# Kernel optimization log

Hardware: AMD Instinct MI355X
Metric: run time of the kernel (lower is better)

The kernel has to match this reference:

```python
import jax, jax.numpy as jnp
import numpy as np

B, S, HID = 2, 2048, 768
NH, HD = 12, 64  # num heads, head dim


def setup_inputs() -> dict:
    key = jax.random.key(0)
    ks = jax.random.split(key, 10)
    scale = 0.02
    return {
        "hidden_states": jax.random.normal(ks[0], (B, S, HID), jnp.float32),
        "rel_pos": jax.random.normal(ks[1], (B, NH, S, S), jnp.float32),
        "rel_2d_pos": jax.random.normal(ks[2], (B, NH, S, S), jnp.float32),
        "attention_mask": jax.random.randint(ks[3], (B, 1, S, S), 0, 2, jnp.int32),
        "Wq": jax.random.normal(ks[4], (HID, HID), jnp.float32) * scale,
        "bq": jnp.zeros((HID,), jnp.float32),
        "Wk": jax.random.normal(ks[5], (HID, HID), jnp.float32) * scale,
        "bk": jnp.zeros((HID,), jnp.float32),
        "Wv": jax.random.normal(ks[6], (HID, HID), jnp.float32) * scale,
        "bv": jnp.zeros((HID,), jnp.float32),
    }


def _heads(x):
    # [B,S,HID] -> [B,NH,S,HD]
    return x.reshape(B, S, NH, HD).transpose(0, 2, 1, 3)


def reference(hidden_states, rel_pos, rel_2d_pos, attention_mask, Wq, bq, Wk, bk, Wv, bv):
    q = _heads(hidden_states @ Wq.T + bq) / jnp.sqrt(jnp.asarray(HD, hidden_states.dtype))
    k = _heads(hidden_states @ Wk.T + bk)
    v = _heads(hidden_states @ Wv.T + bv)
    scores = jnp.einsum('bhsd,bhtd->bhst', q, k)
    scores = scores + rel_pos + rel_2d_pos
    scores = jnp.where(attention_mask.astype(bool), jnp.finfo(jnp.float32).min, scores.astype(jnp.float32))
    probs = jax.nn.softmax(scores, axis=-1).astype(v.dtype)
    ctx = jnp.einsum('bhst,bhtd->bhsd', probs, v)
    return ctx.transpose(0, 2, 1, 3).reshape(B, S, HID)
```

## Files before the change

### kernel.cpp

```cpp
#include <hip/hip_runtime.h>

#define B_ 2
#define S_ 2048
#define HID_ 768
#define NH_ 12
#define HD_ 64
#define NSPLIT 2
#define KSPAN (S_ / NSPLIT)
#define NROWS (B_ * NH_ * S_)

typedef unsigned short u16;
typedef __attribute__((ext_vector_type(8))) short bf16x8;
typedef __attribute__((ext_vector_type(4))) float f32x4;

static __device__ inline u16 f2bf(float f) {
    union { float f; unsigned u; } v; v.f = f;
    unsigned r = v.u + 0x7fffu + ((v.u >> 16) & 1u);
    return (u16)(r >> 16);
}

#define LDS_BARRIER() asm volatile("s_waitcnt lgkmcnt(0)\n\ts_barrier" ::: "memory")

__global__ void cast_bf16(const float* __restrict__ src, u16* __restrict__ dst, int n) {
    int i = (blockIdx.x * blockDim.x + threadIdx.x) * 4;
    if (i < n) {
        float4 v = *(const float4*)(src + i);
        unsigned lo = (unsigned)f2bf(v.x) | ((unsigned)f2bf(v.y) << 16);
        unsigned hi = (unsigned)f2bf(v.z) | ((unsigned)f2bf(v.w) << 16);
        uint2 o; o.x = lo; o.y = hi;
        *(uint2*)(dst + i) = o;
    }
}

__global__ __launch_bounds__(256) void qkv_gemm(
    const u16* __restrict__ hsb, const u16* __restrict__ wcat,
    const float* __restrict__ bq, const float* __restrict__ bk, const float* __restrict__ bv,
    u16* __restrict__ Qg, u16* __restrict__ Kg, u16* __restrict__ Vtg)
{
    __shared__ u16 As[64 * 40];
    __shared__ u16 Bs[64 * 40];
    __shared__ u16 Vs[64 * 72];

    const int m0 = blockIdx.x * 64;
    const int n0 = blockIdx.y * 64;
    const int tid = threadIdx.x;
    const int wave = tid >> 6, lane = tid & 63;
    const int l = lane & 15, quad = lane >> 4;

    f32x4 acc[4];
#pragma unroll
    for (int t = 0; t < 4; t++) acc[t] = (f32x4){0.f, 0.f, 0.f, 0.f};

    const int srow = tid >> 2;
    const int skg = (tid & 3) * 8;

    for (int k0 = 0; k0 < HID_; k0 += 32) {
        *(int4*)(&As[srow * 40 + skg]) = *(const int4*)(&hsb[(size_t)(m0 + srow) * HID_ + k0 + skg]);
        *(int4*)(&Bs[srow * 40 + skg]) = *(const int4*)(&wcat[(size_t)(n0 + srow) * HID_ + k0 + skg]);
        __syncthreads();
        bf16x8 a = *(const bf16x8*)(&As[(wave * 16 + l) * 40 + quad * 8]);
#pragma unroll
        for (int t = 0; t < 4; t++) {
            bf16x8 b = *(const bf16x8*)(&Bs[(t * 16 + l) * 40 + quad * 8]);
            acc[t] = __builtin_amdgcn_mfma_f32_16x16x32_bf16(a, b, acc[t], 0, 0, 0);
        }
        __syncthreads();
    }

    const int proj = n0 / HID_;
    const int cbase = n0 - proj * HID_;
    const int h = cbase >> 6;
    const int bidx = m0 >> 11;
    const int srow0 = m0 & (S_ - 1);
    const float* bias = (proj == 0) ? bq : ((proj == 1) ? bk : bv);

    if (proj < 2) {
        u16* dst = (proj == 0) ? Qg : Kg;
        const float sc = (proj == 0) ? 0.125f : 1.0f;
#pragma unroll
        for (int t = 0; t < 4; t++) {
            const int d = t * 16 + l;
            const float bb = bias[cbase + d];
#pragma unroll
            for (int rr = 0; rr < 4; rr++) {
                int s = srow0 + wave * 16 + quad * 4 + rr;
                float v = (acc[t][rr] + bb) * sc;
                dst[(((size_t)bidx * NH_ + h) * S_ + s) * HD_ + d] = f2bf(v);
            }
        }
    } else {
#pragma unroll
        for (int t = 0; t < 4; t++) {
            const int d = t * 16 + l;
            const float bb = bias[cbase + d];
#pragma unroll
            for (int rr = 0; rr < 4; rr++) {
                int sl = wave * 16 + quad * 4 + rr;
                Vs[d * 72 + sl] = f2bf(acc[t][rr] + bb);
            }
        }
        __syncthreads();
        const int drow = tid >> 2;
        const int sseg = (tid & 3) * 16;
        size_t base = (((size_t)bidx * NH_ + h) * HD_ + drow) * S_ + srow0 + sseg;
        *(int4*)(&Vtg[base])     = *(const int4*)(&Vs[drow * 72 + sseg]);
        *(int4*)(&Vtg[base + 8]) = *(const int4*)(&Vs[drow * 72 + sseg + 8]);
    }
}

__global__ __launch_bounds__(256) void attn(
    const u16* __restrict__ Qg, const u16* __restrict__ Kg, const u16* __restrict__ Vtg,
    const float* __restrict__ rel, const float* __restrict__ rel2,
    const int* __restrict__ mask,
    float* __restrict__ Opart, float* __restrict__ Mpart, float* __restrict__ Lpart)
{
    __shared__ u16 Ks[64 * 72];
    __shared__ u16 Vts[64 * 72];
    __shared__ u16 Ps[4 * 16 * 72];

    const int q0 = blockIdx.x * 64;
    const int h = blockIdx.y;
    const int b = blockIdx.z / NSPLIT;
    const int split = blockIdx.z - b * NSPLIT;
    const int tid = threadIdx.x;
    const int wave = tid >> 6, lane = tid & 63;
    const int l = lane & 15, quad = lane >> 4;
    const int bh = b * NH_ + h;
    const int kbase = split * KSPAN;
    const int kend = kbase + KSPAN;

    const float NEG = -3.4028234663852886e38f;

    bf16x8 qf[2];
    {
        const int qr = q0 + wave * 16 + l;
        qf[0] = *(const bf16x8*)(&Qg[((size_t)bh * S_ + qr) * HD_ + quad * 8]);
        qf[1] = *(const bf16x8*)(&Qg[((size_t)bh * S_ + qr) * HD_ + 32 + quad * 8]);
    }

    f32x4 o[4];
#pragma unroll
    for (int t = 0; t < 4; t++) o[t] = (f32x4){0.f, 0.f, 0.f, 0.f};
    float m_run = NEG, l_run = 0.f;

    const int srow = tid >> 2;
    const int sseg = (tid & 3) * 8;

    const int rsub = lane >> 2;
    const int rcol = (lane & 3) * 4;
    const int rrow = q0 + wave * 16 + rsub;
    const float* relS  = rel  + (size_t)bh * S_ * S_ + (size_t)rrow * S_;
    const float* rel2S = rel2 + (size_t)bh * S_ * S_ + (size_t)rrow * S_;
    const int*   maskS = mask + (size_t)b  * S_ * S_ + (size_t)rrow * S_;
    const int srcLane = 4 * l + quad;

    for (int k0 = kbase; k0 < kend; k0 += 64) {
        size_t kg = ((size_t)bh * S_ + k0 + srow) * HD_;
        int4 ka = *(const int4*)(&Kg[kg + sseg]);
        int4 kb = *(const int4*)(&Kg[kg + 32 + sseg]);
        size_t vg = ((size_t)bh * HD_ + srow) * S_ + k0;
        int4 va = *(const int4*)(&Vtg[vg + sseg]);
        int4 vb = *(const int4*)(&Vtg[vg + 32 + sseg]);

        float4 r[4], s2[4];
        int4 mk[4];
#pragma unroll
        for (int i = 0; i < 4; i++) {
            const int c = k0 + rcol + i * 16;
            r[i]  = *(const float4*)(relS + c);
            s2[i] = *(const float4*)(rel2S + c);
            mk[i] = *(const int4*)(maskS + c);
        }

        *(int4*)(&Ks[srow * 72 + sseg])       = ka;
        *(int4*)(&Ks[srow * 72 + 32 + sseg])  = kb;
        *(int4*)(&Vts[srow * 72 + sseg])      = va;
        *(int4*)(&Vts[srow * 72 + 32 + sseg]) = vb;

        f32x4 ss[4];
#pragma unroll
        for (int i = 0; i < 4; i++) {
            ss[i][0] = mk[i].x ? NEG : r[i].x + s2[i].x;
            ss[i][1] = mk[i].y ? NEG : r[i].y + s2[i].y;
            ss[i][2] = mk[i].z ? NEG : r[i].z + s2[i].z;
            ss[i][3] = mk[i].w ? NEG : r[i].w + s2[i].w;
        }

        f32x4 sacc[4];
#pragma unroll
        for (int t = 0; t < 4; t++) {
            sacc[t][0] = __shfl(ss[t][0], srcLane, 64);
            sacc[t][1] = __shfl(ss[t][1], srcLane, 64);
            sacc[t][2] = __shfl(ss[t][2], srcLane, 64);
            sacc[t][3] = __shfl(ss[t][3], srcLane, 64);
        }

        LDS_BARRIER();

#pragma unroll
        for (int t = 0; t < 4; t++) {
            bf16x8 b0 = *(const bf16x8*)(&Ks[(t * 16 + l) * 72 + quad * 8]);
            sacc[t] = __builtin_amdgcn_mfma_f32_16x16x32_bf16(b0, qf[0], sacc[t], 0, 0, 0);
            bf16x8 b1 = *(const bf16x8*)(&Ks[(t * 16 + l) * 72 + 32 + quad * 8]);
            sacc[t] = __builtin_amdgcn_mfma_f32_16x16x32_bf16(b1, qf[1], sacc[t], 0, 0, 0);
        }

        float mx = NEG;
#pragma unroll
        for (int t = 0; t < 4; t++)
#pragma unroll
            for (int rr = 0; rr < 4; rr++) mx = fmaxf(mx, sacc[t][rr]);
        mx = fmaxf(mx, __shfl_xor(mx, 16, 64));
        mx = fmaxf(mx, __shfl_xor(mx, 32, 64));
        float mnew = fmaxf(m_run, mx);
        float alpha = __expf(m_run - mnew);
        float rs = 0.f;
#pragma unroll
        for (int t = 0; t < 4; t++)
#pragma unroll
            for (int rr = 0; rr < 4; rr++) {
                float p = __expf(sacc[t][rr] - mnew);
                sacc[t][rr] = p;
                rs += p;
            }
        rs += __shfl_xor(rs, 16, 64);
        rs += __shfl_xor(rs, 32, 64);
        l_run = l_run * alpha + rs;
        m_run = mnew;

        float av[4];
#pragma unroll
        for (int rr = 0; rr < 4; rr++) av[rr] = __shfl(alpha, quad * 4 + rr, 64);
#pragma unroll
        for (int dt = 0; dt < 4; dt++)
#pragma unroll
            for (int rr = 0; rr < 4; rr++) o[dt][rr] *= av[rr];

#pragma unroll
        for (int t = 0; t < 4; t++) {
            unsigned p01 = (unsigned)f2bf(sacc[t][0]) | ((unsigned)f2bf(sacc[t][1]) << 16);
            unsigned p23 = (unsigned)f2bf(sacc[t][2]) | ((unsigned)f2bf(sacc[t][3]) << 16);
            uint2 pw; pw.x = p01; pw.y = p23;
            *(uint2*)(&Ps[(wave * 16 + l) * 72 + t * 16 + quad * 4]) = pw;
        }

        bf16x8 pa0 = *(const bf16x8*)(&Ps[(wave * 16 + l) * 72 + quad * 8]);
        bf16x8 pa1 = *(const bf16x8*)(&Ps[(wave * 16 + l) * 72 + 32 + quad * 8]);
#pragma unroll
        for (int dt = 0; dt < 4; dt++) {
            bf16x8 v0 = *(const bf16x8*)(&Vts[(dt * 16 + l) * 72 + quad * 8]);
            o[dt] = __builtin_amdgcn_mfma_f32_16x16x32_bf16(pa0, v0, o[dt], 0, 0, 0);
            bf16x8 v1 = *(const bf16x8*)(&Vts[(dt * 16 + l) * 72 + 32 + quad * 8]);
            o[dt] = __builtin_amdgcn_mfma_f32_16x16x32_bf16(pa1, v1, o[dt], 0, 0, 0);
        }
        LDS_BARRIER();
    }

    float* Op = Opart + (((size_t)split * B_ * NH_ + bh) * S_ + q0) * HD_;
#pragma unroll
    for (int dt = 0; dt < 4; dt++) {
#pragma unroll
        for (int rr = 0; rr < 4; rr++) {
            const int row = wave * 16 + quad * 4 + rr;
            Op[(size_t)row * HD_ + dt * 16 + l] = o[dt][rr];
        }
    }
    if (quad == 0) {
        const size_t mi = ((size_t)split * B_ * NH_ + bh) * S_ + q0 + wave * 16 + l;
        Mpart[mi] = m_run;
        Lpart[mi] = l_run;
    }
}

__global__ __launch_bounds__(256) void combine(
    const float* __restrict__ Op, const float* __restrict__ Mp, const float* __restrict__ Lp,
    float* __restrict__ out)
{
    const int idx = blockIdx.x * 256 + threadIdx.x;
    const int r = idx >> 4;
    const int dseg = (idx & 15) * 4;
    const float m0 = Mp[r], m1 = Mp[NROWS + r];
    const float l0 = Lp[r], l1 = Lp[NROWS + r];
    const float m = fmaxf(m0, m1);
    const float a0 = __expf(m0 - m), a1 = __expf(m1 - m);
    const float inv = 1.0f / (l0 * a0 + l1 * a1);
    const float4 o0 = *(const float4*)(Op + (size_t)r * HD_ + dseg);
    const float4 o1 = *(const float4*)(Op + ((size_t)NROWS + r) * HD_ + dseg);
    float4 res;
    res.x = (o0.x * a0 + o1.x * a1) * inv;
    res.y = (o0.y * a0 + o1.y * a1) * inv;
    res.z = (o0.z * a0 + o1.z * a1) * inv;
    res.w = (o0.w * a0 + o1.w * a1) * inv;
    const int bh_ = r >> 11;
    const int s = r & (S_ - 1);
    const int b = bh_ / NH_;
    const int h = bh_ - b * NH_;
    *(float4*)(out + ((size_t)(b * S_ + s)) * HID_ + h * HD_ + dseg) = res;
}

extern "C" void kernel_launch(void* const* d_in, const int* in_sizes, int n_in,
                              void* d_out, int out_size, void* d_ws, size_t ws_size,
                              hipStream_t stream) {
    const float* hs   = (const float*)d_in[0];
    const float* rel  = (const float*)d_in[1];
    const float* rel2 = (const float*)d_in[2];
    const int*   mask = (const int*)d_in[3];
    const float* Wq = (const float*)d_in[4];
    const float* bq = (const float*)d_in[5];
    const float* Wk = (const float*)d_in[6];
    const float* bk = (const float*)d_in[7];
    const float* Wv = (const float*)d_in[8];
    const float* bv = (const float*)d_in[9];
    float* out = (float*)d_out;

    char* ws = (char*)d_ws;
    u16* hsb   = (u16*)(ws);
    u16* wcat  = (u16*)(ws + 6291456);
    u16* Qg    = (u16*)(ws + 9830400);
    u16* Kg    = (u16*)(ws + 16121856);
    u16* Vtg   = (u16*)(ws + 22413312);
    float* Opart = (float*)(ws + 28704768);
    float* Mpart = (float*)(ws + 53870592);
    float* Lpart = (float*)(ws + 54263808);

    cast_bf16<<<3072, 256, 0, stream>>>(hs, hsb, B_ * S_ * HID_);
    cast_bf16<<<576, 256, 0, stream>>>(Wq, wcat,             HID_ * HID_);
    cast_bf16<<<576, 256, 0, stream>>>(Wk, wcat + HID_ * HID_,     HID_ * HID_);
    cast_bf16<<<576, 256, 0, stream>>>(Wv, wcat + 2 * HID_ * HID_, HID_ * HID_);

    qkv_gemm<<<dim3(64, 36), 256, 0, stream>>>(hsb, wcat, bq, bk, bv, Qg, Kg, Vtg);

    attn<<<dim3(S_ / 64, NH_, B_ * NSPLIT), 256, 0, stream>>>(
        Qg, Kg, Vtg, rel, rel2, mask, Opart, Mpart, Lpart);

    combine<<<(NROWS * 16) / 256, 256, 0, stream>>>(Opart, Mpart, Lpart, out);
}
```

Before: 880.2 us.

## Use single-wave attention blocks reading K/V directly from global memory

The attention kernel goes from 256-thread blocks covering 64 query rows with K/V staged in LDS to 64-thread blocks covering 16 rows. Each wave now loads K and V fragments straight from global memory, which removes both barriers per key tile. It also prefetches the next tile's rel_pos and rel_2d_pos values into registers. In exchange, K/V reuse across the four waves of a block is lost, so global/L2 traffic for K and V rises about fourfold, and the loads are less coalesced.

Measured after the change: 976.3 us. 1.11x slower.

```diff
diff --git a/kernel.cpp b/kernel.cpp
--- a/kernel.cpp
+++ b/kernel.cpp
@@ -19,8 +19,6 @@
     return (u16)(r >> 16);
 }
 
-#define LDS_BARRIER() asm volatile("s_waitcnt lgkmcnt(0)\n\ts_barrier" ::: "memory")
-
 __global__ void cast_bf16(const float* __restrict__ src, u16* __restrict__ dst, int n) {
     int i = (blockIdx.x * blockDim.x + threadIdx.x) * 4;
     if (i < n) {
@@ -108,22 +106,19 @@
     }
 }
 
-__global__ __launch_bounds__(256) void attn(
+__global__ __launch_bounds__(64) void attn(
     const u16* __restrict__ Qg, const u16* __restrict__ Kg, const u16* __restrict__ Vtg,
     const float* __restrict__ rel, const float* __restrict__ rel2,
     const int* __restrict__ mask,
     float* __restrict__ Opart, float* __restrict__ Mpart, float* __restrict__ Lpart)
 {
-    __shared__ u16 Ks[64 * 72];
-    __shared__ u16 Vts[64 * 72];
-    __shared__ u16 Ps[4 * 16 * 72];
-
-    const int q0 = blockIdx.x * 64;
+    __shared__ u16 Ps[16 * 72];
+
+    const int q0 = blockIdx.x * 16;
     const int h = blockIdx.y;
     const int b = blockIdx.z / NSPLIT;
     const int split = blockIdx.z - b * NSPLIT;
-    const int tid = threadIdx.x;
-    const int wave = tid >> 6, lane = tid & 63;
+    const int lane = threadIdx.x;
     const int l = lane & 15, quad = lane >> 4;
     const int bh = b * NH_ + h;
     const int kbase = split * KSPAN;
@@ -131,59 +126,52 @@
 
     const float NEG = -3.4028234663852886e38f;
 
-    bf16x8 qf[2];
-    {
-        const int qr = q0 + wave * 16 + l;
-        qf[0] = *(const bf16x8*)(&Qg[((size_t)bh * S_ + qr) * HD_ + quad * 8]);
-        qf[1] = *(const bf16x8*)(&Qg[((size_t)bh * S_ + qr) * HD_ + 32 + quad * 8]);
-    }
+    const u16* Kbh = Kg + (size_t)bh * S_ * HD_;
+    const u16* Vbh = Vtg + (size_t)bh * HD_ * S_;
+
+    bf16x8 qf0 = *(const bf16x8*)(&Qg[((size_t)bh * S_ + q0 + l) * HD_ + quad * 8]);
+    bf16x8 qf1 = *(const bf16x8*)(&Qg[((size_t)bh * S_ + q0 + l) * HD_ + 32 + quad * 8]);
 
     f32x4 o[4];
 #pragma unroll
     for (int t = 0; t < 4; t++) o[t] = (f32x4){0.f, 0.f, 0.f, 0.f};
     float m_run = NEG, l_run = 0.f;
 
-    const int srow = tid >> 2;
-    const int sseg = (tid & 3) * 8;
-
     const int rsub = lane >> 2;
     const int rcol = (lane & 3) * 4;
-    const int rrow = q0 + wave * 16 + rsub;
-    const float* relS  = rel  + (size_t)bh * S_ * S_ + (size_t)rrow * S_;
-    const float* rel2S = rel2 + (size_t)bh * S_ * S_ + (size_t)rrow * S_;
-    const int*   maskS = mask + (size_t)b  * S_ * S_ + (size_t)rrow * S_;
+    const float* relS  = rel  + (size_t)bh * S_ * S_ + (size_t)(q0 + rsub) * S_;
+    const float* rel2S = rel2 + (size_t)bh * S_ * S_ + (size_t)(q0 + rsub) * S_;
+    const int*   maskS = mask + (size_t)b  * S_ * S_ + (size_t)(q0 + rsub) * S_;
     const int srcLane = 4 * l + quad;
 
+    float4 pr1[4], pr2[4];
+#pragma unroll
+    for (int i = 0; i < 4; i++) {
+        pr1[i] = *(const float4*)(relS + kbase + rcol + i * 16);
+        pr2[i] = *(const float4*)(rel2S + kbase + rcol + i * 16);
+    }
+
     for (int k0 = kbase; k0 < kend; k0 += 64) {
-        size_t kg = ((size_t)bh * S_ + k0 + srow) * HD_;
-        int4 ka = *(const int4*)(&Kg[kg + sseg]);
-        int4 kb = *(const int4*)(&Kg[kg + 32 + sseg]);
-        size_t vg = ((size_t)bh * HD_ + srow) * S_ + k0;
-        int4 va = *(const int4*)(&Vtg[vg + sseg]);
-        int4 vb = *(const int4*)(&Vtg[vg + 32 + sseg]);
-
-        float4 r[4], s2[4];
         int4 mk[4];
 #pragma unroll
+        for (int i = 0; i < 4; i++)
+            mk[i] = *(const int4*)(maskS + k0 + rcol + i * 16);
+
+        f32x4 ss[4];
+#pragma unroll
         for (int i = 0; i < 4; i++) {
-            const int c = k0 + rcol + i * 16;
-            r[i]  = *(const float4*)(relS + c);
-            s2[i] = *(const float4*)(rel2S + c);
-            mk[i] = *(const int4*)(maskS + c);
-        }
-
-        *(int4*)(&Ks[srow * 72 + sseg])       = ka;
-        *(int4*)(&Ks[srow * 72 + 32 + sseg])  = kb;
-        *(int4*)(&Vts[srow * 72 + sseg])      = va;
-        *(int4*)(&Vts[srow * 72 + 32 + sseg]) = vb;
-
-        f32x4 ss[4];
-#pragma unroll
-        for (int i = 0; i < 4; i++) {
-            ss[i][0] = mk[i].x ? NEG : r[i].x + s2[i].x;
-            ss[i][1] = mk[i].y ? NEG : r[i].y + s2[i].y;
-            ss[i][2] = mk[i].z ? NEG : r[i].z + s2[i].z;
-            ss[i][3] = mk[i].w ? NEG : r[i].w + s2[i].w;
+            ss[i][0] = mk[i].x ? NEG : pr1[i].x + pr2[i].x;
+            ss[i][1] = mk[i].y ? NEG : pr1[i].y + pr2[i].y;
+            ss[i][2] = mk[i].z ? NEG : pr1[i].z + pr2[i].z;
+            ss[i][3] = mk[i].w ? NEG : pr1[i].w + pr2[i].w;
+        }
+
+        if (k0 + 64 < kend) {
+#pragma unroll
+            for (int i = 0; i < 4; i++) {
+                pr1[i] = *(const float4*)(relS + k0 + 64 + rcol + i * 16);
+                pr2[i] = *(const float4*)(rel2S + k0 + 64 + rcol + i * 16);
+            }
         }
 
         f32x4 sacc[4];
@@ -195,14 +183,12 @@
             sacc[t][3] = __shfl(ss[t][3], srcLane, 64);
         }
 
-        LDS_BARRIER();
-
-#pragma unroll
-        for (int t = 0; t < 4; t++) {
-            bf16x8 b0 = *(const bf16x8*)(&Ks[(t * 16 + l) * 72 + quad * 8]);
-            sacc[t] = __builtin_amdgcn_mfma_f32_16x16x32_bf16(b0, qf[0], sacc[t], 0, 0, 0);
-            bf16x8 b1 = *(const bf16x8*)(&Ks[(t * 16 + l) * 72 + 32 + quad * 8]);
-            sacc[t] = __builtin_amdgcn_mfma_f32_16x16x32_bf16(b1, qf[1], sacc[t], 0, 0, 0);
+#pragma unroll
+        for (int t = 0; t < 4; t++) {
+            bf16x8 b0 = *(const bf16x8*)(&Kbh[(size_t)(k0 + t * 16 + l) * HD_ + quad * 8]);
+            sacc[t] = __builtin_amdgcn_mfma_f32_16x16x32_bf16(b0, qf0, sacc[t], 0, 0, 0);
+            bf16x8 b1 = *(const bf16x8*)(&Kbh[(size_t)(k0 + t * 16 + l) * HD_ + 32 + quad * 8]);
+            sacc[t] = __builtin_amdgcn_mfma_f32_16x16x32_bf16(b1, qf1, sacc[t], 0, 0, 0);
         }
 
         float mx = NEG;
@@ -241,19 +227,18 @@
             unsigned p01 = (unsigned)f2bf(sacc[t][0]) | ((unsigned)f2bf(sacc[t][1]) << 16);
             unsigned p23 = (unsigned)f2bf(sacc[t][2]) | ((unsigned)f2bf(sacc[t][3]) << 16);
             uint2 pw; pw.x = p01; pw.y = p23;
-            *(uint2*)(&Ps[(wave * 16 + l) * 72 + t * 16 + quad * 4]) = pw;
-        }
-
-        bf16x8 pa0 = *(const bf16x8*)(&Ps[(wave * 16 + l) * 72 + quad * 8]);
-        bf16x8 pa1 = *(const bf16x8*)(&Ps[(wave * 16 + l) * 72 + 32 + quad * 8]);
+            *(uint2*)(&Ps[l * 72 + t * 16 + quad * 4]) = pw;
+        }
+
+        bf16x8 pa0 = *(const bf16x8*)(&Ps[l * 72 + quad * 8]);
+        bf16x8 pa1 = *(const bf16x8*)(&Ps[l * 72 + 32 + quad * 8]);
 #pragma unroll
         for (int dt = 0; dt < 4; dt++) {
-            bf16x8 v0 = *(const bf16x8*)(&Vts[(dt * 16 + l) * 72 + quad * 8]);
+            bf16x8 v0 = *(const bf16x8*)(&Vbh[(size_t)(dt * 16 + l) * S_ + k0 + quad * 8]);
             o[dt] = __builtin_amdgcn_mfma_f32_16x16x32_bf16(pa0, v0, o[dt], 0, 0, 0);
-            bf16x8 v1 = *(const bf16x8*)(&Vts[(dt * 16 + l) * 72 + 32 + quad * 8]);
+            bf16x8 v1 = *(const bf16x8*)(&Vbh[(size_t)(dt * 16 + l) * S_ + k0 + 32 + quad * 8]);
             o[dt] = __builtin_amdgcn_mfma_f32_16x16x32_bf16(pa1, v1, o[dt], 0, 0, 0);
         }
-        LDS_BARRIER();
     }
 
     float* Op = Opart + (((size_t)split * B_ * NH_ + bh) * S_ + q0) * HD_;
@@ -261,12 +246,12 @@
     for (int dt = 0; dt < 4; dt++) {
 #pragma unroll
         for (int rr = 0; rr < 4; rr++) {
-            const int row = wave * 16 + quad * 4 + rr;
+            const int row = quad * 4 + rr;
             Op[(size_t)row * HD_ + dt * 16 + l] = o[dt][rr];
         }
     }
     if (quad == 0) {
-        const size_t mi = ((size_t)split * B_ * NH_ + bh) * S_ + q0 + wave * 16 + l;
+        const size_t mi = ((size_t)split * B_ * NH_ + bh) * S_ + q0 + l;
         Mpart[mi] = m_run;
         Lpart[mi] = l_run;
     }
@@ -330,7 +315,7 @@
 
     qkv_gemm<<<dim3(64, 36), 256, 0, stream>>>(hsb, wcat, bq, bk, bv, Qg, Kg, Vtg);
 
-    attn<<<dim3(S_ / 64, NH_, B_ * NSPLIT), 256, 0, stream>>>(
+    attn<<<dim3(S_ / 16, NH_, B_ * NSPLIT), 64, 0, stream>>>(
         Qg, Kg, Vtg, rel, rel2, mask, Opart, Mpart, Lpart);
 
     combine<<<(NROWS * 16) / 256, 256, 0, stream>>>(Opart, Mpart, Lpart, out);
```
